# Kernel tuning notes

Hardware: AMD Instinct MI355X
Metric: run time of the kernel (lower is better)

## Reference

```python
import jax, jax.numpy as jnp
import numpy as np

EPS = 1e-5
GRID = 128          # coarse grid extent -> fine grid is 256^3
N1 = 15000          # coarse voxels
CHILD = 4           # children kept per coarse voxel
N2 = N1 * CHILD     # fine voxels
CIN = 128
COUT = 64


def _build_geometry():
    rng = np.random.RandomState(0)
    flat = rng.choice(GRID ** 3, N1, replace=False)
    cc = np.stack(np.unravel_index(flat, (GRID, GRID, GRID)), axis=1)  # [N1,3]
    offs8 = np.array([[i, j, k] for i in (0, 1) for j in (0, 1) for k in (0, 1)], dtype=np.int64)
    kidx = np.argsort(rng.rand(N1, 8), axis=1)[:, :CHILD]              # [N1,4] distinct child taps
    fine = (cc[:, None, :] * 2 + offs8[kidx]).reshape(-1, 3)           # [N2,3] unique fine coords
    up_src = np.repeat(np.arange(N1), CHILD).astype(np.int32)
    up_kidx = kidx.reshape(-1).astype(np.int32)
    # 27-offset neighbor maps via hashed coordinate lookup
    key = (fine[:, 0] * 256 + fine[:, 1]) * 256 + fine[:, 2]
    order = np.argsort(key)
    skey = key[order]
    offs27 = np.array([[i, j, k] for i in (-1, 0, 1) for j in (-1, 0, 1) for k in (-1, 0, 1)], dtype=np.int64)
    nbr_src = np.full((27, N2), N2, dtype=np.int32)
    nbr_dst = np.full((27, N2), N2, dtype=np.int32)
    for t in range(27):
        q = fine + offs27[t]
        inb = np.all((q >= 0) & (q < 256), axis=1)
        qk = (q[:, 0] * 256 + q[:, 1]) * 256 + q[:, 2]
        pos = np.searchsorted(skey, qk)
        pos = np.clip(pos, 0, N2 - 1)
        hit = inb & (skey[pos] == qk)
        nbr_src[t, hit] = order[pos[hit]]
        nbr_dst[t, hit] = np.arange(N2, dtype=np.int32)[hit]
    return up_src, up_kidx, nbr_src, nbr_dst


def setup_inputs() -> dict:
    key = jax.random.key(0)
    ks = jax.random.split(key, 8)
    up_src, up_kidx, nbr_src, nbr_dst = _build_geometry()
    s_up = 1.0 / np.sqrt(CIN * 8)
    s1 = 1.0 / np.sqrt(CIN * 27)
    s2 = 1.0 / np.sqrt(COUT * 27)
    return {
        "feats1": jax.random.normal(ks[0], (N1, CIN), jnp.float32),
        "feats2": jax.random.normal(ks[1], (N2, CIN // 2), jnp.float32),
        "w_up": jax.random.normal(ks[2], (8, CIN, CIN // 2), jnp.float32) * s_up,
        "gamma_up": jnp.ones((CIN // 2,), jnp.float32),
        "beta_up": jnp.zeros((CIN // 2,), jnp.float32),
        "w1": jax.random.normal(ks[3], (27, CIN, COUT), jnp.float32) * s1,
        "gamma1": jnp.ones((COUT,), jnp.float32),
        "beta1": jnp.zeros((COUT,), jnp.float32),
        "w2": jax.random.normal(ks[4], (27, COUT, COUT), jnp.float32) * s2,
        "gamma2": jnp.ones((COUT,), jnp.float32),
        "beta2": jnp.zeros((COUT,), jnp.float32),
        "up_src": jnp.asarray(up_src),
        "up_kidx": jnp.asarray(up_kidx),
        "nbr_src": jnp.asarray(nbr_src),
        "nbr_dst": jnp.asarray(nbr_dst),
    }


def _bn_relu(x, gamma, beta):
    # training-mode BatchNorm over the point dimension (biased variance), then ReLU
    m = jnp.mean(x, axis=0)
    v = jnp.var(x, axis=0)
    return jax.nn.relu((x - m) * jax.lax.rsqrt(v + EPS) * gamma + beta)


def _sparse_conv(x, w, nbr_src, nbr_dst):
    # x: [N,Ci]; w: [27,Ci,Co]; transform-then-gather-scatter (hash-map sparse conv)
    n = x.shape[0]
    co = w.shape[-1]
    y = jnp.einsum("nc,kco->kno", x, w)                       # [27,N,Co]
    y = jnp.concatenate([y, jnp.zeros((27, 1, co), y.dtype)], axis=1)  # sentinel row
    msg = jnp.take_along_axis(y, nbr_src[:, :, None], axis=1)  # [27,N,Co]
    out = jnp.zeros((n + 1, co), y.dtype).at[nbr_dst.reshape(-1)].add(msg.reshape(-1, co))
    return out[:-1]


def reference(feats1, feats2, w_up, gamma_up, beta_up, w1, gamma1, beta1, w2,
              gamma2, beta2, up_src, up_kidx, nbr_src, nbr_dst):
    # transposed conv k=2 s=2, generative=False: each fine voxel pulls from its unique coarse parent
    y = jnp.einsum("mc,kco->kmo", feats1, w_up)               # [8,N1,Cin/2]
    x1 = y[up_kidx, up_src]                                   # [N2,Cin/2]
    x1 = _bn_relu(x1, gamma_up, beta_up)
    x = jnp.concatenate([x1, feats2], axis=-1)                # [N2,Cin]
    h = _bn_relu(_sparse_conv(x, w1, nbr_src, nbr_dst), gamma1, beta1)
    return _bn_relu(_sparse_conv(h, w2, nbr_src, nbr_dst), gamma2, beta2)
```

## Files before the change

kernel.cpp:

```cpp
#include <hip/hip_runtime.h>


typedef short bf16x4 __attribute__((ext_vector_type(4)));
typedef short bf16x8 __attribute__((ext_vector_type(8)));
typedef float f32x16 __attribute__((ext_vector_type(16)));

__device__ __forceinline__ short f2bf(float f) {
    unsigned u = __float_as_uint(f);
    u += 0x7fffu + ((u >> 16) & 1u);
    return (short)(u >> 16);
}
__device__ __forceinline__ float bf2f(short s) {
    return __uint_as_float(((unsigned)(unsigned short)s) << 16);
}

__global__ __launch_bounds__(256) void k_setup(
    const float* __restrict__ w_up, const float* __restrict__ w1,
    const float* __restrict__ w2, const float* __restrict__ f1,
    const int* __restrict__ nbr, const int* __restrict__ up_kidx,
    short* __restrict__ wupp, short* __restrict__ w1p,
    short* __restrict__ w2p, short* __restrict__ f1bf,
    int* __restrict__ pmask, int* __restrict__ perm_rows,
    int* __restrict__ rank, int* __restrict__ cnt,
    int2* __restrict__ ext, int* __restrict__ extc,
    float* __restrict__ y1, float* __restrict__ y2,
    int n1, int n2, int nbExt, int nbGeom)
{
    int tid = threadIdx.x;
    int bid = blockIdx.x;
    if (bid < nbExt) {
        long long tot = (long long)n2 * 16;
        long long gs = (long long)nbExt * 256;
        for (long long e = (long long)bid * 256 + tid; e < tot; e += gs) {
            ((float4*)y1)[e] = make_float4(0.f, 0.f, 0.f, 0.f);
            ((float4*)y2)[e] = make_float4(0.f, 0.f, 0.f, 0.f);
        }
        int i = bid * 256 + tid;
        unsigned hm = 0;
        if (i < n2) {
            #pragma unroll
            for (int t = 0; t < 27; ++t) {
                int s = nbr[(size_t)t * n2 + i];
                if (s < n2 && (s >> 2) != (i >> 2)) hm |= 1u << t;
            }
        }
        __shared__ int lcnt, lbase;
        if (tid == 0) lcnt = 0;
        __syncthreads();
        int nh = __popc(hm);
        int myofs = 0;
        if (nh) myofs = atomicAdd(&lcnt, nh);
        __syncthreads();
        if (tid == 0 && lcnt) lbase = atomicAdd(extc, lcnt);
        __syncthreads();
        if (nh) {
            int pos = lbase + myofs;
            unsigned m = hm;
            while (m) {
                int t = __ffs(m) - 1;
                m &= m - 1;
                int s = nbr[(size_t)t * n2 + i];
                ext[pos++] = make_int2(i, s | (t << 16));
            }
        }
    } else if (bid < nbExt + nbGeom) {
        int p = (bid - nbExt) * 256 + tid;
        if (p >= n1) return;
        int4 kd = *(const int4*)(up_kidx + 4 * p);
        int a = kd.x * 4 + 0, b = kd.y * 4 + 1, c = kd.z * 4 + 2, d = kd.w * 4 + 3;
        int t;
        if (a > b) { t = a; a = b; b = t; }
        if (c > d) { t = c; c = d; d = t; }
        if (a > c) { t = a; a = c; c = t; }
        if (b > d) { t = b; b = d; d = t; }
        if (b > c) { t = b; b = c; c = t; }
        perm_rows[4 * p + 0] = 4 * p + (a & 3);
        perm_rows[4 * p + 1] = 4 * p + (b & 3);
        perm_rows[4 * p + 2] = 4 * p + (c & 3);
        perm_rows[4 * p + 3] = 4 * p + (d & 3);
        int mask = (1 << (a >> 2)) | (1 << (b >> 2)) | (1 << (c >> 2)) | (1 << (d >> 2));
        pmask[p] = mask;
        rank[p] = atomicAdd(&cnt[mask], 1);
    } else {
        const long long nup = 65536, nw1 = 221184, nw2 = 110592;
        long long nf1 = (long long)n1 * 128;
        long long total = nup + nw1 + nw2 + nf1;
        long long gs = (long long)(gridDim.x - nbExt - nbGeom) * 256;
        for (long long e0 = (long long)(bid - nbExt - nbGeom) * 256 + tid;
             e0 < total; e0 += gs) {
            long long e = e0;
            if (e < nup) {
                int j = e & 7, l = (e >> 3) & 63, nt = (e >> 9) & 15, ks = (int)(e >> 13);
                int k = ks * 16 + (l >> 5) * 8 + j;
                int col = nt * 32 + (l & 31);
                wupp[e] = f2bf(w_up[((size_t)(col >> 6) * 128 + k) * 64 + (col & 63)]);
            } else if ((e -= nup) < nw1) {
                int j = e & 7, l = (e >> 3) & 63, ch = (e >> 9) & 1, ks = (e >> 10) & 7, t = (int)(e >> 13);
                int k = ks * 16 + (l >> 5) * 8 + j;
                int col = ch * 32 + (l & 31);
                w1p[e] = f2bf(w1[((size_t)t * 128 + k) * 64 + col]);
            } else if ((e -= nw1) < nw2) {
                int j = e & 7, l = (e >> 3) & 63, ch = (e >> 9) & 1, ks = (e >> 10) & 3, t = (int)(e >> 12);
                int k = ks * 16 + (l >> 5) * 8 + j;
                int col = ch * 32 + (l & 31);
                w2p[e] = f2bf(w2[((size_t)t * 64 + k) * 64 + col]);
            } else {
                e -= nw2;
                f1bf[e] = f2bf(f1[e]);
            }
        }
    }
}

__global__ __launch_bounds__(256) void k_up(
    const short* __restrict__ f1bf, const short* __restrict__ wupp,
    const int* __restrict__ pmask, const int* __restrict__ cnt,
    const int* __restrict__ rank, int* __restrict__ perm_par,
    int4* __restrict__ tiles, int* __restrict__ ntl,
    short* __restrict__ yup8, float* __restrict__ stats, int n1)
{
    if (blockIdx.x == 0) {
        __shared__ int sA[256], sB[256], bb[256];
        int t = threadIdx.x;
        int c = cnt[t], tc = (c + 31) >> 5;
        sA[t] = c; sB[t] = tc;
        __syncthreads();
        for (int off = 1; off < 256; off <<= 1) {
            int a = (t >= off) ? sA[t - off] : 0;
            int b = (t >= off) ? sB[t - off] : 0;
            __syncthreads();
            sA[t] += a; sB[t] += b;
            __syncthreads();
        }
        int base = sA[t] - c, toff = sB[t] - tc;
        bb[t] = base;
        for (int j = 0; j < tc; ++j) tiles[toff + j] = make_int4(t, base, j * 32, c);
        if (t == 255) ntl[0] = sB[255];
        __syncthreads();
        for (int p = t; p < n1; p += 256)
            perm_par[bb[pmask[p]] + rank[p]] = p;
        return;
    }
    __shared__ short lds[32 * 136];
    __shared__ float bs[64], bq[64];
    int bid = blockIdx.x - 1;
    int tile = bid >> 1;
    int w = threadIdx.x >> 6, lane = threadIdx.x & 63;
    int na = (bid & 1) * 8 + w, nb = na + 4;
    if (threadIdx.x < 64) { bs[threadIdx.x] = 0.f; bq[threadIdx.x] = 0.f; }
    #pragma unroll
    for (int it = 0; it < 2; ++it) {
        int c = it * 256 + threadIdx.x;
        int row = c >> 4, col8 = c & 15;
        int gr = tile * 32 + row; if (gr >= n1) gr = n1 - 1;
        int4 g = *(const int4*)(f1bf + (size_t)gr * 128 + col8 * 8);
        short* d = &lds[row * 136 + col8 * 8];
        *(int2*)d = make_int2(g.x, g.y);
        *(int2*)(d + 4) = make_int2(g.z, g.w);
    }
    int m = lane & 31, half = lane >> 5;
    int pm_l = (tile * 32 + m < n1) ? pmask[tile * 32 + m] : 0;
    __syncthreads();
    f32x16 a0, a1;
    #pragma unroll
    for (int i = 0; i < 16; ++i) { a0[i] = 0.f; a1[i] = 0.f; }
    const bf16x8* bp = (const bf16x8*)wupp;
    #pragma unroll
    for (int ks = 0; ks < 8; ++ks) {
        const short* ap = &lds[m * 136 + ks * 16 + half * 8];
        bf16x4 lo = *(const bf16x4*)ap, hi = *(const bf16x4*)(ap + 4);
        bf16x8 a = __builtin_shufflevector(lo, hi, 0, 1, 2, 3, 4, 5, 6, 7);
        bf16x8 b0 = bp[(size_t)(ks * 16 + na) * 64 + lane];
        bf16x8 b1 = bp[(size_t)(ks * 16 + nb) * 64 + lane];
        a0 = __builtin_amdgcn_mfma_f32_32x32x16_bf16(a, b0, a0, 0, 0, 0);
        a1 = __builtin_amdgcn_mfma_f32_32x32x16_bf16(a, b1, a1, 0, 0, 0);
    }
    int col = lane & 31;
    #pragma unroll
    for (int pass = 0; pass < 2; ++pass) {
        const f32x16& acc = pass ? a1 : a0;
        int n = pass ? nb : na;
        int slot = n >> 1, c = (n & 1) * 32 + col;
        float s0 = 0.f, q0 = 0.f;
        #pragma unroll
        for (int reg = 0; reg < 16; ++reg) {
            int r = (reg & 3) + 8 * (reg >> 2) + 4 * half;
            int p = tile * 32 + r;
            float v = acc[reg];
            int mk = __shfl(pm_l, r);
            if (p < n1) {
                yup8[(size_t)p * 512 + n * 32 + col] = f2bf(v);
                if ((mk >> slot) & 1) { s0 += v; q0 += v * v; }
            }
        }
        s0 += __shfl_xor(s0, 32);
        q0 += __shfl_xor(q0, 32);
        if (lane < 32) { atomicAdd(&bs[c], s0); atomicAdd(&bq[c], q0); }
    }
    __syncthreads();
    if (threadIdx.x < 64) {
        atomicAdd(&stats[threadIdx.x], bs[threadIdx.x]);
        atomicAdd(&stats[64 + threadIdx.x], bq[threadIdx.x]);
    }
}

__global__ __launch_bounds__(256) void k_extA(
    const short* __restrict__ yup8, const float* __restrict__ f2,
    const int* __restrict__ up_kidx, const float* __restrict__ w1,
    const float* __restrict__ gamma, const float* __restrict__ beta,
    const float* __restrict__ stats, const int2* __restrict__ ext,
    const int* __restrict__ extc, float* __restrict__ y, int n2)
{
    __shared__ float sc[64], sh[64];
    int tid = threadIdx.x;
    if (tid < 64) {
        float inv = 1.0f / (float)n2;
        float mean = stats[tid] * inv;
        float var = stats[64 + tid] * inv - mean * mean;
        float s = gamma[tid] * rsqrtf(var + 1e-5f);
        sc[tid] = s; sh[tid] = beta[tid] - mean * s;
    }
    __syncthreads();
    int gw = (blockIdx.x * 256 + tid) >> 6;
    int nw = (gridDim.x * 256) >> 6;
    int c = tid & 63;
    int ec = extc[0];
    for (int e = gw; e < ec; e += nw) {
        int2 en = ext[e];
        int i = en.x, s = en.y & 0xFFFF, t = en.y >> 16;
        const short* xr = yup8 + (size_t)(s >> 2) * 512 + up_kidx[s] * 64;
        const float* fr = f2 + (size_t)s * 64;
        const float* wr = w1 + (size_t)t * 8192 + c;
        float acc = 0.f;
        #pragma unroll 4
        for (int k = 0; k < 64; ++k) {
            float xk = fmaxf(bf2f(xr[k]) * sc[k] + sh[k], 0.f);
            acc += xk * wr[(size_t)k * 64];
        }
        #pragma unroll 4
        for (int k = 0; k < 64; ++k)
            acc += fr[k] * wr[(size_t)(64 + k) * 64];
        atomicAdd(&y[(size_t)i * 64 + c], acc);
    }
}

__global__ __launch_bounds__(256) void k_extB(
    const float* __restrict__ y1, const float* __restrict__ w2,
    const float* __restrict__ gamma, const float* __restrict__ beta,
    const float* __restrict__ stats, const int2* __restrict__ ext,
    const int* __restrict__ extc, float* __restrict__ y, int n2)
{
    __shared__ float sc[64], sh[64];
    int tid = threadIdx.x;
    if (tid < 64) {
        float inv = 1.0f / (float)n2;
        float mean = stats[tid] * inv;
        float var = stats[64 + tid] * inv - mean * mean;
        float s = gamma[tid] * rsqrtf(var + 1e-5f);
        sc[tid] = s; sh[tid] = beta[tid] - mean * s;
    }
    __syncthreads();
    int gw = (blockIdx.x * 256 + tid) >> 6;
    int nw = (gridDim.x * 256) >> 6;
    int c = tid & 63;
    int ec = extc[0];
    for (int e = gw; e < ec; e += nw) {
        int2 en = ext[e];
        int i = en.x, s = en.y & 0xFFFF, t = en.y >> 16;
        const float* hr = y1 + (size_t)s * 64;
        const float* wr = w2 + (size_t)t * 4096 + c;
        float acc = 0.f;
        #pragma unroll 4
        for (int k = 0; k < 64; ++k) {
            float hk = fmaxf(hr[k] * sc[k] + sh[k], 0.f);
            acc += hk * wr[(size_t)k * 64];
        }
        atomicAdd(&y[(size_t)i * 64 + c], acc);
    }
}

__device__ __forceinline__ void pair_epi2(const f32x16& a0v, const f32x16& a1v,
                                          int outrow0, int outrow1, int lane,
                                          int ch, float* __restrict__ y,
                                          float* __restrict__ bs,
                                          float* __restrict__ bq)
{
    int col = lane & 31;
    int c = ch * 32 + col;
    int r0[16], r1[16];
    #pragma unroll
    for (int reg = 0; reg < 16; ++reg) {
        int r = (reg & 3) + 8 * (reg >> 2) + 4 * (lane >> 5);
        r0[reg] = __shfl(outrow0, r);
        r1[reg] = __shfl(outrow1, r);
    }
    float o0[16], o1[16];
    #pragma unroll
    for (int reg = 0; reg < 16; ++reg) {
        int ra = (r0[reg] >= 0) ? r0[reg] : 0;
        int rb = (r1[reg] >= 0) ? r1[reg] : 0;
        o0[reg] = y[(size_t)ra * 64 + c];
        o1[reg] = y[(size_t)rb * 64 + c];
    }
    float s0 = 0.f, q0 = 0.f;
    #pragma unroll
    for (int reg = 0; reg < 16; ++reg) {
        if (r0[reg] >= 0) {
            float v = a0v[reg] + o0[reg];
            y[(size_t)r0[reg] * 64 + c] = v;
            s0 += v; q0 += v * v;
        }
        if (r1[reg] >= 0) {
            float v = a1v[reg] + o1[reg];
            y[(size_t)r1[reg] * 64 + c] = v;
            s0 += v; q0 += v * v;
        }
    }
    s0 += __shfl_xor(s0, 32);
    q0 += __shfl_xor(q0, 32);
    if (lane < 32) { atomicAdd(&bs[c], s0); atomicAdd(&bq[c], q0); }
}

__device__ __forceinline__ int tap27(int pa, int pb) {
    int di = ((pb >> 2) & 1) - ((pa >> 2) & 1);
    int dj = ((pb >> 1) & 1) - ((pa >> 1) & 1);
    int dk = (pb & 1) - (pa & 1);
    return (di + 1) * 9 + (dj + 1) * 3 + (dk + 1);
}

__global__ __launch_bounds__(256) void k_pairA(
    const short* __restrict__ yup8, const float* __restrict__ f2,
    const int* __restrict__ up_kidx, const short* __restrict__ wp,
    const float* __restrict__ gamma, const float* __restrict__ beta,
    const float* __restrict__ stats, const int* __restrict__ perm_par,
    const int* __restrict__ perm_rows, const int4* __restrict__ tiles,
    const int* __restrict__ n_tiles, float* __restrict__ y,
    float* __restrict__ ostats, int n2)
{
    constexpr int LP = 520;
    __shared__ short lds[32 * LP];
    __shared__ int srows[128], soff[128];
    __shared__ float scs[64], shs[64], bs[64], bq[64];
    int bt = blockIdx.x;
    if (bt >= n_tiles[0]) return;
    int4 td = tiles[bt];
    int mask = td.x, p_start = td.y, lt = td.z, cntb = td.w;
    int tid = threadIdx.x;
    if (tid < 128) {
        int li = lt + (tid >> 2);
        int pid = perm_par[p_start + ((li < cntb) ? li : 0)];
        int i = perm_rows[pid * 4 + (tid & 3)];
        srows[tid] = i;
        soff[tid] = (i >> 2) * 512 + up_kidx[i] * 64;
    } else if (tid < 192) {
        int cc = tid - 128;
        float inv = 1.0f / (float)n2;
        float mean = stats[cc] * inv;
        float var = stats[64 + cc] * inv - mean * mean;
        float s = gamma[cc] * rsqrtf(var + 1e-5f);
        scs[cc] = s; shs[cc] = beta[cc] - mean * s;
    } else {
        int cc = tid - 192;
        bs[cc] = 0.f; bq[cc] = 0.f;
    }
    __syncthreads();
    #pragma unroll
    for (int it = 0; it < 8; ++it) {
        int c0 = it * 256 + tid;
        int pl = c0 >> 6, w8 = c0 & 63;
        int j = w8 >> 4, col8 = w8 & 15;
        short* d = &lds[pl * LP + j * 128 + col8 * 8];
        if (col8 < 8) {
            bf16x8 g = *(const bf16x8*)(yup8 + (size_t)soff[pl * 4 + j] + col8 * 8);
            short o[8];
            #pragma unroll
            for (int u = 0; u < 8; ++u) {
                int cc = col8 * 8 + u;
                o[u] = f2bf(fmaxf(bf2f(g[u]) * scs[cc] + shs[cc], 0.f));
            }
            *(int2*)d = make_int2(((int)(unsigned short)o[0]) | ((int)o[1] << 16),
                                  ((int)(unsigned short)o[2]) | ((int)o[3] << 16));
            *(int2*)(d + 4) = make_int2(((int)(unsigned short)o[4]) | ((int)o[5] << 16),
                                        ((int)(unsigned short)o[6]) | ((int)o[7] << 16));
        } else {
            const float* fr = f2 + (size_t)srows[pl * 4 + j] * 64 + (col8 - 8) * 8;
            float4 f0 = *(const float4*)fr;
            float4 f1v = *(const float4*)(fr + 4);
            short o[8] = {f2bf(f0.x), f2bf(f0.y), f2bf(f0.z), f2bf(f0.w),
                          f2bf(f1v.x), f2bf(f1v.y), f2bf(f1v.z), f2bf(f1v.w)};
            *(int2*)d = make_int2(((int)(unsigned short)o[0]) | ((int)o[1] << 16),
                                  ((int)(unsigned short)o[2]) | ((int)o[3] << 16));
            *(int2*)(d + 4) = make_int2(((int)(unsigned short)o[4]) | ((int)o[5] << 16),
                                        ((int)(unsigned short)o[6]) | ((int)o[7] << 16));
        }
    }
    int p0 = -1, p1 = -1, p2 = -1, p3 = -1;
    #pragma unroll
    for (int b = 7; b >= 0; --b)
        if ((mask >> b) & 1) { p3 = p2; p2 = p1; p1 = p0; p0 = b; }
    int w = tid >> 6, lane = tid & 63;
    int a0 = w >> 1, a1 = a0 + 2, ch = w & 1;
    int pa0 = (a0 == 0) ? p0 : p1;
    int pa1 = (a1 == 2) ? p2 : p3;
    int t00 = tap27(pa0, p0), t01 = tap27(pa0, p1), t02 = tap27(pa0, p2), t03 = tap27(pa0, p3);
    int t10 = tap27(pa1, p0), t11 = tap27(pa1, p1), t12 = tap27(pa1, p2), t13 = tap27(pa1, p3);
    int m = lane & 31, half = lane >> 5;
    int li = lt + m;
    bool vp = li < cntb;
    int pid = perm_par[p_start + (vp ? li : 0)];
    int outrow0 = vp ? perm_rows[pid * 4 + a0] : -1;
    int outrow1 = vp ? perm_rows[pid * 4 + a1] : -1;
    __syncthreads();
    f32x16 acc0, acc1;
    #pragma unroll
    for (int i = 0; i < 16; ++i) { acc0[i] = 0.f; acc1[i] = 0.f; }
    const bf16x8* bp = (const bf16x8*)wp;
    #pragma unroll
    for (int b = 0; b < 4; ++b) {
        int tb0 = (b == 0) ? t00 : (b == 1) ? t01 : (b == 2) ? t02 : t03;
        int tb1 = (b == 0) ? t10 : (b == 1) ? t11 : (b == 2) ? t12 : t13;
        #pragma unroll
        for (int kk = 0; kk < 8; ++kk) {
            int ks = b * 8 + kk;
            const short* ap = &lds[m * LP + ks * 16 + half * 8];
            bf16x4 lo = *(const bf16x4*)ap, hi = *(const bf16x4*)(ap + 4);
            bf16x8 a = __builtin_shufflevector(lo, hi, 0, 1, 2, 3, 4, 5, 6, 7);
            bf16x8 b0 = bp[((size_t)(tb0 * 8 + kk) * 2 + ch) * 64 + lane];
            bf16x8 b1 = bp[((size_t)(tb1 * 8 + kk) * 2 + ch) * 64 + lane];
            acc0 = __builtin_amdgcn_mfma_f32_32x32x16_bf16(a, b0, acc0, 0, 0, 0);
            acc1 = __builtin_amdgcn_mfma_f32_32x32x16_bf16(a, b1, acc1, 0, 0, 0);
        }
    }
    pair_epi2(acc0, acc1, outrow0, outrow1, lane, ch, y, bs, bq);
    __syncthreads();
    if (tid < 64) {
        atomicAdd(&ostats[tid], bs[tid]);
        atomicAdd(&ostats[64 + tid], bq[tid]);
    }
}

__global__ __launch_bounds__(256) void k_pairB(
    const float* __restrict__ y1, const short* __restrict__ wp,
    const float* __restrict__ gamma, const float* __restrict__ beta,
    const float* __restrict__ stats, const int* __restrict__ perm_par,
    const int* __restrict__ perm_rows, const int4* __restrict__ tiles,
    const int* __restrict__ n_tiles, float* __restrict__ y,
    float* __restrict__ ostats, int n2)
{
    constexpr int LP = 264;
    __shared__ short lds[32 * LP];
    __shared__ int srows[128];
    __shared__ float scs[64], shs[64], bs[64], bq[64];
    int bt = blockIdx.x;
    if (bt >= n_tiles[0]) return;
    int4 td = tiles[bt];
    int mask = td.x, p_start = td.y, lt = td.z, cntb = td.w;
    int tid = threadIdx.x;
    if (tid < 128) {
        int li = lt + (tid >> 2);
        int pid = perm_par[p_start + ((li < cntb) ? li : 0)];
        srows[tid] = perm_rows[pid * 4 + (tid & 3)];
    } else if (tid < 192) {
        int cc = tid - 128;
        float inv = 1.0f / (float)n2;
        float mean = stats[cc] * inv;
        float var = stats[64 + cc] * inv - mean * mean;
        float s = gamma[cc] * rsqrtf(var + 1e-5f);
        scs[cc] = s; shs[cc] = beta[cc] - mean * s;
    } else {
        int cc = tid - 192;
        bs[cc] = 0.f; bq[cc] = 0.f;
    }
    __syncthreads();
    #pragma unroll
    for (int it = 0; it < 4; ++it) {
        int c0 = it * 256 + tid;
        int pl = c0 >> 5, w8 = c0 & 31;
        int j = w8 >> 3, col8 = w8 & 7;
        const float* fr = y1 + (size_t)srows[pl * 4 + j] * 64 + col8 * 8;
        float4 f0 = *(const float4*)fr;
        float4 f1v = *(const float4*)(fr + 4);
        short o[8];
        #pragma unroll
        for (int u = 0; u < 4; ++u) {
            int cc = col8 * 8 + u;
            float v = (u == 0) ? f0.x : (u == 1) ? f0.y : (u == 2) ? f0.z : f0.w;
            o[u] = f2bf(fmaxf(v * scs[cc] + shs[cc], 0.f));
        }
        #pragma unroll
        for (int u = 0; u < 4; ++u) {
            int cc = col8 * 8 + 4 + u;
            float v = (u == 0) ? f1v.x : (u == 1) ? f1v.y : (u == 2) ? f1v.z : f1v.w;
            o[4 + u] = f2bf(fmaxf(v * scs[cc] + shs[cc], 0.f));
        }
        short* d = &lds[pl * LP + j * 64 + col8 * 8];
        *(int2*)d = make_int2(((int)(unsigned short)o[0]) | ((int)o[1] << 16),
                              ((int)(unsigned short)o[2]) | ((int)o[3] << 16));
        *(int2*)(d + 4) = make_int2(((int)(unsigned short)o[4]) | ((int)o[5] << 16),
                                    ((int)(unsigned short)o[6]) | ((int)o[7] << 16));
    }
    int p0 = -1, p1 = -1, p2 = -1, p3 = -1;
    #pragma unroll
    for (int b = 7; b >= 0; --b)
        if ((mask >> b) & 1) { p3 = p2; p2 = p1; p1 = p0; p0 = b; }
    int w = tid >> 6, lane = tid & 63;
    int a0 = w >> 1, a1 = a0 + 2, ch = w & 1;
    int pa0 = (a0 == 0) ? p0 : p1;
    int pa1 = (a1 == 2) ? p2 : p3;
    int t00 = tap27(pa0, p0), t01 = tap27(pa0, p1), t02 = tap27(pa0, p2), t03 = tap27(pa0, p3);
    int t10 = tap27(pa1, p0), t11 = tap27(pa1, p1), t12 = tap27(pa1, p2), t13 = tap27(pa1, p3);
    int m = lane & 31, half = lane >> 5;
    int li = lt + m;
    bool vp = li < cntb;
    int pid = perm_par[p_start + (vp ? li : 0)];
    int outrow0 = vp ? perm_rows[pid * 4 + a0] : -1;
    int outrow1 = vp ? perm_rows[pid * 4 + a1] : -1;
    __syncthreads();
    f32x16 acc0, acc1;
    #pragma unroll
    for (int i = 0; i < 16; ++i) { acc0[i] = 0.f; acc1[i] = 0.f; }
    const bf16x8* bp = (const bf16x8*)wp;
    #pragma unroll
    for (int b = 0; b < 4; ++b) {
        int tb0 = (b == 0) ? t00 : (b == 1) ? t01 : (b == 2) ? t02 : t03;
        int tb1 = (b == 0) ? t10 : (b == 1) ? t11 : (b == 2) ? t12 : t13;
        #pragma unroll
        for (int kk = 0; kk < 4; ++kk) {
            int ks = b * 4 + kk;
            const short* ap = &lds[m * LP + ks * 16 + half * 8];
            bf16x4 lo = *(const bf16x4*)ap, hi = *(const bf16x4*)(ap + 4);
            bf16x8 a = __builtin_shufflevector(lo, hi, 0, 1, 2, 3, 4, 5, 6, 7);
            bf16x8 b0 = bp[((size_t)(tb0 * 4 + kk) * 2 + ch) * 64 + lane];
            bf16x8 b1 = bp[((size_t)(tb1 * 4 + kk) * 2 + ch) * 64 + lane];
            acc0 = __builtin_amdgcn_mfma_f32_32x32x16_bf16(a, b0, acc0, 0, 0, 0);
            acc1 = __builtin_amdgcn_mfma_f32_32x32x16_bf16(a, b1, acc1, 0, 0, 0);
        }
    }
    pair_epi2(acc0, acc1, outrow0, outrow1, lane, ch, y, bs, bq);
    __syncthreads();
    if (tid < 64) {
        atomicAdd(&ostats[tid], bs[tid]);
        atomicAdd(&ostats[64 + tid], bq[tid]);
    }
}

__global__ __launch_bounds__(256) void k_final(
    const float* __restrict__ y, const float* __restrict__ gamma,
    const float* __restrict__ beta, const float* __restrict__ stats,
    float* __restrict__ out, int n2)
{
    __shared__ float sc[64], sh[64];
    int tid = threadIdx.x;
    if (tid < 64) {
        float inv = 1.0f / (float)n2;
        float mean = stats[tid] * inv;
        float var = stats[64 + tid] * inv - mean * mean;
        float s = gamma[tid] * rsqrtf(var + 1e-5f);
        sc[tid] = s;
        sh[tid] = beta[tid] - mean * s;
    }
    __syncthreads();
    long long total = (long long)n2 * 16;
    long long stride = (long long)gridDim.x * blockDim.x;
    for (long long idx = (long long)blockIdx.x * blockDim.x + tid; idx < total; idx += stride) {
        int i = (int)(idx >> 4);
        int c4 = ((int)idx & 15) * 4;
        const float* src = y + (size_t)i * 64 + c4;
        float4 o;
        o.x = fmaxf(src[0] * sc[c4 + 0] + sh[c4 + 0], 0.f);
        o.y = fmaxf(src[1] * sc[c4 + 1] + sh[c4 + 1], 0.f);
        o.z = fmaxf(src[2] * sc[c4 + 2] + sh[c4 + 2], 0.f);
        o.w = fmaxf(src[3] * sc[c4 + 3] + sh[c4 + 3], 0.f);
        *(float4*)(out + (size_t)i * 64 + c4) = o;
    }
}

extern "C" void kernel_launch(void* const* d_in, const int* in_sizes, int n_in,
                              void* d_out, int out_size, void* d_ws, size_t ws_size,
                              hipStream_t stream)
{
    const float* feats1   = (const float*)d_in[0];
    const float* feats2   = (const float*)d_in[1];
    const float* w_up     = (const float*)d_in[2];
    const float* gamma_up = (const float*)d_in[3];
    const float* beta_up  = (const float*)d_in[4];
    const float* w1       = (const float*)d_in[5];
    const float* gamma1   = (const float*)d_in[6];
    const float* beta1    = (const float*)d_in[7];
    const float* w2       = (const float*)d_in[8];
    const float* gamma2   = (const float*)d_in[9];
    const float* beta2    = (const float*)d_in[10];
    const int* up_src     = (const int*)d_in[11];  (void)up_src;
    const int* up_kidx    = (const int*)d_in[12];
    const int* nbr_src    = (const int*)d_in[13];

    int n1 = in_sizes[0] / 128;
    int n2 = in_sizes[1] / 64;

    char* p = (char*)d_ws;
    auto alloc = [&](size_t bytes) {
        char* r = p;
        p += (bytes + 255) & ~(size_t)255;
        return r;
    };
    float* stats    = (float*)alloc(384 * 4);
    int*   cnt      = (int*)alloc(256 * 4);
    int*   extc     = (int*)alloc(16);
    int*   ntl      = (int*)alloc(16);
    size_t headBytes = (size_t)(p - (char*)d_ws);
    int maxTiles    = (n1 + 31) / 32 + 80;
    int4*  tiles    = (int4*)alloc((size_t)maxTiles * 16);
    short* wupp     = (short*)alloc((size_t)65536 * 2);
    short* w1p      = (short*)alloc((size_t)221184 * 2);
    short* w2p      = (short*)alloc((size_t)110592 * 2);
    short* f1bf     = (short*)alloc((size_t)n1 * 128 * 2);
    int*   pmask    = (int*)alloc((size_t)n1 * 4);
    int*   rank     = (int*)alloc((size_t)n1 * 4);
    int*   perm_par = (int*)alloc((size_t)n1 * 4);
    int*   perm_rows= (int*)alloc((size_t)4 * n1 * 4);
    int2*  ext      = (int2*)alloc((size_t)27 * n2 * 8);
    short* yup8     = (short*)alloc((size_t)n1 * 512 * 2);
    float* y1       = (float*)alloc((size_t)n2 * 64 * 4);
    float* y2       = (float*)alloc((size_t)n2 * 64 * 4);

    int nbExt  = (n2 + 255) / 256;
    int nbGeom = (n1 + 255) / 256;
    int nbPack = 256;
    int nbSetup = nbExt + nbGeom + nbPack;
    int upBlocks = 1 + 2 * ((n1 + 31) / 32);
    int ewBlocks16 = (int)(((long long)n2 * 16 + 255) / 256);

    hipMemsetAsync(d_ws, 0, headBytes, stream);
    k_setup<<<nbSetup, 256, 0, stream>>>(w_up, w1, w2, feats1, nbr_src, up_kidx,
                                         wupp, w1p, w2p, f1bf, pmask, perm_rows,
                                         rank, cnt, ext, extc, y1, y2,
                                         n1, n2, nbExt, nbGeom);
    k_up<<<upBlocks, 256, 0, stream>>>(f1bf, wupp, pmask, cnt, rank, perm_par,
                                       tiles, ntl, yup8, stats, n1);
    k_extA<<<512, 256, 0, stream>>>(yup8, feats2, up_kidx, w1, gamma_up, beta_up,
                                    stats, ext, extc, y1, n2);
    k_pairA<<<maxTiles, 256, 0, stream>>>(yup8, feats2, up_kidx, w1p, gamma_up,
                                          beta_up, stats, perm_par, perm_rows,
                                          tiles, ntl, y1, stats + 128, n2);
    k_extB<<<512, 256, 0, stream>>>(y1, w2, gamma1, beta1, stats + 128, ext,
                                    extc, y2, n2);
    k_pairB<<<maxTiles, 256, 0, stream>>>(y1, w2p, gamma1, beta1, stats + 128,
                                          perm_par, perm_rows, tiles, ntl, y2,
                                          stats + 256, n2);
    k_final<<<ewBlocks16, 256, 0, stream>>>(y2, gamma2, beta2, stats + 256,
                                            (float*)d_out, n2);
}
```

Baseline: 245.6 us.

## Move ext-list build, y zeroing and conv weight packing into k_up launch

Shrinks k_setup to the geometry sort and the packing of w_up and feats1, so the upsample GEMM can start earlier. The neighbor ext-list construction, the y1/y2 zeroing and the w1/w2 bf16 packing now run as extra blocks of k_up, alongside the upsample GEMM tiles. Weight and feature packing is also vectorized to write 8 bf16 values per thread with a single 16-byte store. This trades a longer k_setup critical path for independent work overlapping with the GEMM, at the cost of a larger k_up grid.

Result: faster. 237.6 us (-3.3%).

```diff
diff --git a/kernel.cpp b/kernel.cpp
--- a/kernel.cpp
+++ b/kernel.cpp
@@ -15,56 +15,17 @@
 }
 
 __global__ __launch_bounds__(256) void k_setup(
-    const float* __restrict__ w_up, const float* __restrict__ w1,
-    const float* __restrict__ w2, const float* __restrict__ f1,
-    const int* __restrict__ nbr, const int* __restrict__ up_kidx,
-    short* __restrict__ wupp, short* __restrict__ w1p,
-    short* __restrict__ w2p, short* __restrict__ f1bf,
+    const float* __restrict__ w_up, const float* __restrict__ f1,
+    const int* __restrict__ up_kidx,
+    short* __restrict__ wupp, short* __restrict__ f1bf,
     int* __restrict__ pmask, int* __restrict__ perm_rows,
     int* __restrict__ rank, int* __restrict__ cnt,
-    int2* __restrict__ ext, int* __restrict__ extc,
-    float* __restrict__ y1, float* __restrict__ y2,
-    int n1, int n2, int nbExt, int nbGeom)
+    int n1, int nbGeom)
 {
     int tid = threadIdx.x;
     int bid = blockIdx.x;
-    if (bid < nbExt) {
-        long long tot = (long long)n2 * 16;
-        long long gs = (long long)nbExt * 256;
-        for (long long e = (long long)bid * 256 + tid; e < tot; e += gs) {
-            ((float4*)y1)[e] = make_float4(0.f, 0.f, 0.f, 0.f);
-            ((float4*)y2)[e] = make_float4(0.f, 0.f, 0.f, 0.f);
-        }
-        int i = bid * 256 + tid;
-        unsigned hm = 0;
-        if (i < n2) {
-            #pragma unroll
-            for (int t = 0; t < 27; ++t) {
-                int s = nbr[(size_t)t * n2 + i];
-                if (s < n2 && (s >> 2) != (i >> 2)) hm |= 1u << t;
-            }
-        }
-        __shared__ int lcnt, lbase;
-        if (tid == 0) lcnt = 0;
-        __syncthreads();
-        int nh = __popc(hm);
-        int myofs = 0;
-        if (nh) myofs = atomicAdd(&lcnt, nh);
-        __syncthreads();
-        if (tid == 0 && lcnt) lbase = atomicAdd(extc, lcnt);
-        __syncthreads();
-        if (nh) {
-            int pos = lbase + myofs;
-            unsigned m = hm;
-            while (m) {
-                int t = __ffs(m) - 1;
-                m &= m - 1;
-                int s = nbr[(size_t)t * n2 + i];
-                ext[pos++] = make_int2(i, s | (t << 16));
-            }
-        }
-    } else if (bid < nbExt + nbGeom) {
-        int p = (bid - nbExt) * 256 + tid;
+    if (bid < nbGeom) {
+        int p = bid * 256 + tid;
         if (p >= n1) return;
         int4 kd = *(const int4*)(up_kidx + 4 * p);
         int a = kd.x * 4 + 0, b = kd.y * 4 + 1, c = kd.z * 4 + 2, d = kd.w * 4 + 3;
@@ -82,31 +43,28 @@
         pmask[p] = mask;
         rank[p] = atomicAdd(&cnt[mask], 1);
     } else {
-        const long long nup = 65536, nw1 = 221184, nw2 = 110592;
-        long long nf1 = (long long)n1 * 128;
-        long long total = nup + nw1 + nw2 + nf1;
-        long long gs = (long long)(gridDim.x - nbExt - nbGeom) * 256;
-        for (long long e0 = (long long)(bid - nbExt - nbGeom) * 256 + tid;
-             e0 < total; e0 += gs) {
-            long long e = e0;
-            if (e < nup) {
-                int j = e & 7, l = (e >> 3) & 63, nt = (e >> 9) & 15, ks = (int)(e >> 13);
-                int k = ks * 16 + (l >> 5) * 8 + j;
+        const int nup8 = 8192;
+        int tot = nup8 + n1 * 16;
+        int gs = (gridDim.x - nbGeom) * 256;
+        for (int e8 = (bid - nbGeom) * 256 + tid; e8 < tot; e8 += gs) {
+            if (e8 < nup8) {
+                int l = e8 & 63, nt = (e8 >> 6) & 15, ks = e8 >> 10;
+                int kb = ks * 16 + (l >> 5) * 8;
                 int col = nt * 32 + (l & 31);
-                wupp[e] = f2bf(w_up[((size_t)(col >> 6) * 128 + k) * 64 + (col & 63)]);
-            } else if ((e -= nup) < nw1) {
-                int j = e & 7, l = (e >> 3) & 63, ch = (e >> 9) & 1, ks = (e >> 10) & 7, t = (int)(e >> 13);
-                int k = ks * 16 + (l >> 5) * 8 + j;
-                int col = ch * 32 + (l & 31);
-                w1p[e] = f2bf(w1[((size_t)t * 128 + k) * 64 + col]);
-            } else if ((e -= nw1) < nw2) {
-                int j = e & 7, l = (e >> 3) & 63, ch = (e >> 9) & 1, ks = (e >> 10) & 3, t = (int)(e >> 12);
-                int k = ks * 16 + (l >> 5) * 8 + j;
-                int col = ch * 32 + (l & 31);
-                w2p[e] = f2bf(w2[((size_t)t * 64 + k) * 64 + col]);
+                const float* src = w_up + (size_t)(col >> 6) * 8192 + (size_t)kb * 64 + (col & 63);
+                bf16x8 o;
+                #pragma unroll
+                for (int j = 0; j < 8; ++j) o[j] = f2bf(src[(size_t)j * 64]);
+                *(bf16x8*)(wupp + (size_t)e8 * 8) = o;
             } else {
-                e -= nw2;
-                f1bf[e] = f2bf(f1[e]);
+                int g = e8 - nup8;
+                const float* src = f1 + (size_t)g * 8;
+                float4 a = *(const float4*)src;
+                float4 b = *(const float4*)(src + 4);
+                bf16x8 o;
+                o[0] = f2bf(a.x); o[1] = f2bf(a.y); o[2] = f2bf(a.z); o[3] = f2bf(a.w);
+                o[4] = f2bf(b.x); o[5] = f2bf(b.y); o[6] = f2bf(b.z); o[7] = f2bf(b.w);
+                *(bf16x8*)(f1bf + (size_t)g * 8) = o;
             }
         }
     }
@@ -117,8 +75,14 @@
     const int* __restrict__ pmask, const int* __restrict__ cnt,
     const int* __restrict__ rank, int* __restrict__ perm_par,
     int4* __restrict__ tiles, int* __restrict__ ntl,
-    short* __restrict__ yup8, float* __restrict__ stats, int n1)
-{
+    short* __restrict__ yup8, float* __restrict__ stats,
+    const float* __restrict__ w1, const float* __restrict__ w2,
+    short* __restrict__ w1p, short* __restrict__ w2p,
+    const int* __restrict__ nbr, int2* __restrict__ ext,
+    int* __restrict__ extc, float* __restrict__ y1, float* __restrict__ y2,
+    int n1, int n2, int nt, int nbExt)
+{
+    int gemmEnd = 1 + 2 * nt;
     if (blockIdx.x == 0) {
         __shared__ int sA[256], sB[256], bb[256];
         int t = threadIdx.x;
@@ -139,6 +103,72 @@
         __syncthreads();
         for (int p = t; p < n1; p += 256)
             perm_par[bb[pmask[p]] + rank[p]] = p;
+        return;
+    }
+    if (blockIdx.x >= gemmEnd) {
+        int ab = blockIdx.x - gemmEnd;
+        int tid = threadIdx.x;
+        if (ab < 256) {
+            long long tot = (long long)n2 * 16;
+            float4 z = make_float4(0.f, 0.f, 0.f, 0.f);
+            for (long long e = (long long)ab * 256 + tid; e < tot; e += 256LL * 256) {
+                ((float4*)y1)[e] = z;
+                ((float4*)y2)[e] = z;
+            }
+        } else if (ab < 320) {
+            const int nw18 = 27648, tot = 27648 + 13824;
+            for (int e8 = (ab - 256) * 256 + tid; e8 < tot; e8 += 64 * 256) {
+                if (e8 < nw18) {
+                    int l = e8 & 63, ch = (e8 >> 6) & 1, ks = (e8 >> 7) & 7, t = e8 >> 10;
+                    int kb = ks * 16 + (l >> 5) * 8;
+                    int col = ch * 32 + (l & 31);
+                    const float* src = w1 + (size_t)t * 8192 + (size_t)kb * 64 + col;
+                    bf16x8 o;
+                    #pragma unroll
+                    for (int j = 0; j < 8; ++j) o[j] = f2bf(src[(size_t)j * 64]);
+                    *(bf16x8*)(w1p + (size_t)e8 * 8) = o;
+                } else {
+                    int g = e8 - nw18;
+                    int l = g & 63, ch = (g >> 6) & 1, ks = (g >> 7) & 3, t = g >> 9;
+                    int kb = ks * 16 + (l >> 5) * 8;
+                    int col = ch * 32 + (l & 31);
+                    const float* src = w2 + (size_t)t * 4096 + (size_t)kb * 64 + col;
+                    bf16x8 o;
+                    #pragma unroll
+                    for (int j = 0; j < 8; ++j) o[j] = f2bf(src[(size_t)j * 64]);
+                    *(bf16x8*)(w2p + (size_t)g * 8) = o;
+                }
+            }
+        } else {
+            int i = (ab - 320) * 256 + tid;
+            unsigned hm = 0;
+            if (i < n2) {
+                #pragma unroll
+                for (int t = 0; t < 27; ++t) {
+                    int s = nbr[(size_t)t * n2 + i];
+                    if (s < n2 && (s >> 2) != (i >> 2)) hm |= 1u << t;
+                }
+            }
+            __shared__ int lcnt, lbase;
+            if (tid == 0) lcnt = 0;
+            __syncthreads();
+            int nh = __popc(hm);
+            int myofs = 0;
+            if (nh) myofs = atomicAdd(&lcnt, nh);
+            __syncthreads();
+            if (tid == 0 && lcnt) lbase = atomicAdd(extc, lcnt);
+            __syncthreads();
+            if (nh) {
+                int pos = lbase + myofs;
+                unsigned m = hm;
+                while (m) {
+                    int t = __ffs(m) - 1;
+                    m &= m - 1;
+                    int s = nbr[(size_t)t * n2 + i];
+                    ext[pos++] = make_int2(i, s | (t << 16));
+                }
+            }
+        }
         return;
     }
     __shared__ short lds[32 * 136];
@@ -625,18 +655,20 @@
 
     int nbExt  = (n2 + 255) / 256;
     int nbGeom = (n1 + 255) / 256;
-    int nbPack = 256;
-    int nbSetup = nbExt + nbGeom + nbPack;
-    int upBlocks = 1 + 2 * ((n1 + 31) / 32);
+    int nbPack = 128;
+    int nbSetup = nbGeom + nbPack;
+    int nt = (n1 + 31) / 32;
+    int upBlocks = 1 + 2 * nt + 256 + 64 + nbExt;
     int ewBlocks16 = (int)(((long long)n2 * 16 + 255) / 256);
 
     hipMemsetAsync(d_ws, 0, headBytes, stream);
-    k_setup<<<nbSetup, 256, 0, stream>>>(w_up, w1, w2, feats1, nbr_src, up_kidx,
-                                         wupp, w1p, w2p, f1bf, pmask, perm_rows,
-                                         rank, cnt, ext, extc, y1, y2,
-                                         n1, n2, nbExt, nbGeom);
+    k_setup<<<nbSetup, 256, 0, stream>>>(w_up, feats1, up_kidx, wupp, f1bf,
+                                         pmask, perm_rows, rank, cnt,
+                                         n1, nbGeom);
     k_up<<<upBlocks, 256, 0, stream>>>(f1bf, wupp, pmask, cnt, rank, perm_par,
-                                       tiles, ntl, yup8, stats, n1);
+                                       tiles, ntl, yup8, stats,
+                                       w1, w2, w1p, w2p, nbr_src, ext, extc,
+                                       y1, y2, n1, n2, nt, nbExt);
     k_extA<<<512, 256, 0, stream>>>(yup8, feats2, up_kidx, w1, gamma_up, beta_up,
                                     stats, ext, extc, y1, n2);
     k_pairA<<<maxTiles, 256, 0, stream>>>(yup8, feats2, up_kidx, w1p, gamma_up,
```
